# Optimization experiments

Measured on AMD Instinct MI355X. Metric: run time of the kernel, lower is better.

## Reference

```python
import jax, jax.numpy as jnp
import numpy as np
import math

D_MODEL = 1024
D_STATE = 16
D_CONV = 4
EXPAND = 2
D_INNER = EXPAND * D_MODEL  # 2048
DT_RANK = 64
B_SZ = 2
L_SEQ = 1024


def setup_inputs() -> dict:
    key = jax.random.key(0)
    ks = jax.random.split(key, 10)
    x = jax.random.normal(ks[0], (B_SZ, L_SEQ, D_MODEL), dtype=jnp.float32)
    in_proj_w = jax.random.normal(ks[1], (2 * D_INNER, D_MODEL), dtype=jnp.float32) * (1.0 / math.sqrt(D_MODEL))
    conv_w = jax.random.normal(ks[2], (D_INNER, 1, D_CONV), dtype=jnp.float32) * (1.0 / math.sqrt(D_CONV))
    conv_b = jax.random.normal(ks[3], (D_INNER,), dtype=jnp.float32) * 0.01
    x_proj_w = jax.random.normal(ks[4], (DT_RANK + 2 * D_STATE, D_INNER), dtype=jnp.float32) * (1.0 / math.sqrt(D_INNER))
    dt_init_std = DT_RANK ** (-0.5)
    dt_proj_w = jax.random.uniform(ks[5], (D_INNER, DT_RANK), dtype=jnp.float32, minval=-dt_init_std, maxval=dt_init_std)
    dt = jnp.exp(jax.random.uniform(ks[6], (D_INNER,), dtype=jnp.float32) * (math.log(0.1) - math.log(0.001)) + math.log(0.001))
    dt = jnp.clip(dt, 1e-4, None)
    dt_proj_b = dt + jnp.log(-jnp.expm1(-dt))
    A_log = jnp.log(jnp.tile(jnp.arange(1, D_STATE + 1, dtype=jnp.float32)[None, :], (D_INNER, 1)))
    D = jnp.ones((D_INNER,), dtype=jnp.float32)
    out_proj_w = jax.random.normal(ks[7], (D_MODEL, D_INNER), dtype=jnp.float32) * (1.0 / math.sqrt(D_INNER))
    return {"x": x, "in_proj_w": in_proj_w, "conv_w": conv_w, "conv_b": conv_b,
            "x_proj_w": x_proj_w, "dt_proj_w": dt_proj_w, "dt_proj_b": dt_proj_b,
            "A_log": A_log, "D": D, "out_proj_w": out_proj_w}


def _mamba_forward(x, in_proj_w, conv_w, conv_b, x_proj_w, dt_proj_w, dt_proj_b, A_log, D, out_proj_w):
    B, L, _ = x.shape
    # input projection -> x, z each [B, L, Di]
    xz = jnp.einsum('bld,ed->ble', x, in_proj_w)
    xs, z = jnp.split(xz, 2, axis=-1)
    # causal depthwise conv along L (torch pads K-1 both sides then trims -> left pad only)
    xc = jnp.transpose(xs, (0, 2, 1))  # [B, Di, L]
    xc = jax.lax.conv_general_dilated(
        xc, conv_w, window_strides=(1,), padding=[(D_CONV - 1, 0)],
        feature_group_count=D_INNER, dimension_numbers=('NCH', 'OIH', 'NCH'))
    xc = xc + conv_b[None, :, None]
    xs = jnp.transpose(xc, (0, 2, 1))  # [B, L, Di]
    xs = jax.nn.silu(xs)
    # SSM parameters
    A = -jnp.exp(A_log)  # [Di, N]
    dbc = jnp.einsum('bld,ed->ble', xs, x_proj_w)
    delta_r = dbc[..., :DT_RANK]
    Bm = dbc[..., DT_RANK:DT_RANK + D_STATE]       # [B, L, N]
    Cm = dbc[..., DT_RANK + D_STATE:]              # [B, L, N]
    delta = jnp.einsum('blr,dr->bld', delta_r, dt_proj_w)
    delta = jax.nn.softplus(delta + dt_proj_b)     # [B, L, Di]
    # selective scan: h_t = exp(delta*A)*h_{t-1} + delta*B*x
    dA = jnp.exp(delta[..., None] * A)                          # [B, L, Di, N]
    dBx = (delta * xs)[..., None] * Bm[:, :, None, :]           # [B, L, Di, N]
    dA_t = jnp.moveaxis(dA, 1, 0)    # [L, B, Di, N]
    dBx_t = jnp.moveaxis(dBx, 1, 0)
    C_t = jnp.moveaxis(Cm, 1, 0)     # [L, B, N]
    h0 = jnp.zeros((B, D_INNER, D_STATE), dtype=xs.dtype)

    def step(h, inp):
        da, bx, c = inp
        h = da * h + bx
        y = jnp.einsum('bdn,bn->bd', h, c)
        return h, y

    _, ys = jax.lax.scan(step, h0, (dA_t, dBx_t, C_t))
    y = jnp.moveaxis(ys, 0, 1)       # [B, L, Di]
    y = y + D * xs
    # gating and output projection
    out = y * jax.nn.silu(z)
    return jnp.einsum('bld,od->blo', out, out_proj_w)


def reference(x, in_proj_w, conv_w, conv_b, x_proj_w, dt_proj_w, dt_proj_b, A_log, D, out_proj_w):
    return _mamba_forward(x, in_proj_w, conv_w, conv_b, x_proj_w, dt_proj_w, dt_proj_b, A_log, D, out_proj_w)
```

## Files before the change

### kernel.cpp

```cpp
#include <hip/hip_runtime.h>
#include <hip/hip_bf16.h>

typedef __attribute__((ext_vector_type(8))) short short8;
typedef __attribute__((ext_vector_type(4))) float f32x4;
typedef __hip_bfloat16 bf16;

#define D_MODEL 1024
#define D_INNER 2048
#define DT_RANK 64
#define D_STATE 16
#define B_SZ 2
#define L_SEQ 1024
#define NSEG 32
#define SL 32

__device__ __forceinline__ float b2f(bf16 x){ return __bfloat162float(x); }
__device__ __forceinline__ bf16  f2b(float x){ return __float2bfloat16(x); }

__device__ __forceinline__ void cvt_store8(bf16* dst, const float* s){
  union { short8 v; bf16 e[8]; } u;
  #pragma unroll
  for (int i = 0; i < 8; i++) u.e[i] = f2b(s[i]);
  *(short8*)dst = u.v;
}

__device__ __forceinline__ void gl_lds16(const bf16* g, bf16* l){
  __builtin_amdgcn_global_load_lds((const __attribute__((address_space(1))) unsigned int*)g,
                                   (__attribute__((address_space(3))) unsigned int*)l, 16, 0, 0);
}

__global__ __launch_bounds__(256) void cvt5_k(const float* s0, bf16* d0, int c0,
                                              const float* s1, bf16* d1, int c1,
                                              const float* s2, bf16* d2, int c2,
                                              const float* s3, bf16* d3, int c3,
                                              const float* s4, bf16* d4, int c4)
{
  int i = blockIdx.x * 256 + threadIdx.x;
  const float* s; bf16* d; int off;
  if      (i < c0) { s = s0; d = d0; off = i; }
  else if (i < c1) { s = s1; d = d1; off = i - c0; }
  else if (i < c2) { s = s2; d = d2; off = i - c1; }
  else if (i < c3) { s = s3; d = d3; off = i - c2; }
  else if (i < c4) { s = s4; d = d4; off = i - c3; }
  else return;
  float b[8];
  *(float4*)&b[0] = *(const float4*)(s + (size_t)off * 8);
  *(float4*)&b[4] = *(const float4*)(s + (size_t)off * 8 + 4);
  cvt_store8(d + (size_t)off * 8, b);
}

template<int MODE, int JT>
__global__ __launch_bounds__(256) void gemm_glds(const bf16* __restrict__ A,
                                                 const bf16* __restrict__ B,
                                                 void* __restrict__ Cout,
                                                 int M, int N, int K)
{
  constexpr int BN = JT * 32;
  constexpr int BI = BN / 64;
  constexpr int ES = (MODE == 0) ? 4 : 2;
  static_assert(BN * ES == 256, "copy-out assumes 256B tile rows");
  constexpr int ROWB = BN * ES + 16;
  constexpr int STAGE_AB = 128*32*2 + BN*32*2;
  constexpr int SMEM = (128 * ROWB > STAGE_AB) ? 128 * ROWB : STAGE_AB;
  __shared__ __align__(16) char smem[SMEM];
  bf16* As = (bf16*)smem;
  bf16* Bs = (bf16*)(smem + 128*32*2);

  const int bm = blockIdx.y * 128, bn = blockIdx.x * BN;
  const int tid  = threadIdx.x;
  const int lane = tid & 63, wave = tid >> 6;
  const int wm = (wave & 1) * 64, wn = (wave >> 1) * (JT * 16);
  const int r = lane & 15, q = lane >> 4;

  const bf16* asrc[2];
  #pragma unroll
  for (int i = 0; i < 2; i++) {
    int c = i * 256 + tid;
    asrc[i] = A + (size_t)(bm + (c >> 2)) * K + (c & 3) * 8;
  }
  const bf16* bsrc[BI];
  #pragma unroll
  for (int i = 0; i < BI; i++) {
    int c = i * 256 + tid;
    bsrc[i] = B + (size_t)(bn + (c >> 2)) * K + (c & 3) * 8;
  }

  f32x4 acc[4][JT];
  #pragma unroll
  for (int i = 0; i < 4; i++)
    #pragma unroll
    for (int j = 0; j < JT; j++) acc[i][j] = (f32x4){0.f,0.f,0.f,0.f};

  for (int k0 = 0; k0 < K; k0 += 32) {
    #pragma unroll
    for (int i = 0; i < 2; i++)
      gl_lds16(asrc[i] + k0, &As[(i * 256 + tid) * 8]);
    #pragma unroll
    for (int i = 0; i < BI; i++)
      gl_lds16(bsrc[i] + k0, &Bs[(i * 256 + tid) * 8]);
    __syncthreads();
    short8 af[4], bfr[JT];
    #pragma unroll
    for (int i = 0; i < 4; i++)  af[i]  = *(const short8*)&As[(wm + i*16 + r) * 32 + q*8];
    #pragma unroll
    for (int j = 0; j < JT; j++) bfr[j] = *(const short8*)&Bs[(wn + j*16 + r) * 32 + q*8];
    #pragma unroll
    for (int j = 0; j < JT; j++)
      #pragma unroll
      for (int i = 0; i < 4; i++)
        acc[i][j] = __builtin_amdgcn_mfma_f32_16x16x32_bf16(af[i], bfr[j], acc[i][j], 0, 0, 0);
    __syncthreads();
  }

  #pragma unroll
  for (int i = 0; i < 4; i++)
    #pragma unroll
    for (int j = 0; j < JT; j++)
      #pragma unroll
      for (int t = 0; t < 4; t++) {
        int lrow = wm + i*16 + q*4 + t;
        int lcol = wn + j*16 + r;
        float v = acc[i][j][t];
        if (MODE == 0) *(float*)(smem + lrow*ROWB + lcol*4) = v;
        else           *(bf16*)(smem + lrow*ROWB + lcol*2) = f2b(v);
      }
  __syncthreads();
  {
    int row0 = tid >> 3, ch = tid & 7;
    #pragma unroll
    for (int rr = 0; rr < 4; rr++) {
      int row = row0 + rr * 32;
      const char* src = smem + row*ROWB + ch*32;
      float4 w0 = *(const float4*)src;
      float4 w1 = *(const float4*)(src + 16);
      char* gdst = (char*)Cout + ((size_t)(bm + row) * N + bn) * ES + ch*32;
      *(float4*)gdst        = w0;
      *(float4*)(gdst + 16) = w1;
    }
  }
}

__global__ __launch_bounds__(256) void gemm_dt(const bf16* __restrict__ A,
                                               const bf16* __restrict__ W,
                                               float* __restrict__ Cout,
                                               const float* __restrict__ bias,
                                               int M, int N)
{
  __shared__ __align__(16) float stg[4][16][68];
  const int lane = threadIdx.x & 63, wave = threadIdx.x >> 6;
  const int ntg  = N >> 6;
  const int task = blockIdx.x * 4 + wave;
  const int mt   = task / ntg;
  const int ng   = task - mt * ntg;
  const int r = lane & 15, q = lane >> 4;

  const bf16* pa = A + (size_t)(mt*16 + r) * DT_RANK + q*8;
  short8 a0 = *(const short8*)pa;
  short8 a1 = *(const short8*)(pa + 32);

  #pragma unroll
  for (int j = 0; j < 4; j++) {
    const bf16* pb = W + (size_t)(ng*64 + j*16 + r) * DT_RANK + q*8;
    short8 b0 = *(const short8*)pb;
    short8 b1 = *(const short8*)(pb + 32);
    f32x4 c = {0.f,0.f,0.f,0.f};
    c = __builtin_amdgcn_mfma_f32_16x16x32_bf16(a0, b0, c, 0, 0, 0);
    c = __builtin_amdgcn_mfma_f32_16x16x32_bf16(a1, b1, c, 0, 0, 0);
    float bv = bias[ng*64 + j*16 + r];
    #pragma unroll
    for (int t = 0; t < 4; t++) {
      float xv = c[t] + bv;
      float sp = (xv > 20.f) ? xv : log1pf(__expf(xv));
      stg[wave][q*4 + t][j*16 + r] = sp;
    }
  }
  {
    int row = lane >> 2, q4 = lane & 3;
    const float* src = &stg[wave][row][q4 * 16];
    float4 w0 = *(const float4*)(src);
    float4 w1 = *(const float4*)(src + 4);
    float4 w2 = *(const float4*)(src + 8);
    float4 w3 = *(const float4*)(src + 12);
    float* gdst = Cout + (size_t)(mt*16 + row) * N + ng*64 + q4*16;
    *(float4*)(gdst)      = w0;
    *(float4*)(gdst + 4)  = w1;
    *(float4*)(gdst + 8)  = w2;
    *(float4*)(gdst + 12) = w3;
  }
}

__global__ __launch_bounds__(256) void gemm_xproj(const bf16* __restrict__ A,
                                                  const bf16* __restrict__ W,
                                                  float* __restrict__ dbc,
                                                  bf16* __restrict__ dr)
{
  const int K = D_INNER;
  const int lane = threadIdx.x & 63, wave = threadIdx.x >> 6;
  const int mt = blockIdx.y * 4 + wave;
  const int nt = blockIdx.x;
  const int r = lane & 15, q = lane >> 4;
  const bf16* pa = A + (size_t)(mt*16 + r) * K + q*8;
  const bf16* pb = W + (size_t)(nt*16 + r) * K + q*8;
  f32x4 a0 = {0.f,0.f,0.f,0.f}, a1 = a0, a2 = a0, a3 = a0;
  for (int k0 = 0; k0 < K; k0 += 128) {
    short8 x0 = *(const short8*)(pa + k0);
    short8 w0 = *(const short8*)(pb + k0);
    short8 x1 = *(const short8*)(pa + k0 + 32);
    short8 w1 = *(const short8*)(pb + k0 + 32);
    short8 x2 = *(const short8*)(pa + k0 + 64);
    short8 w2 = *(const short8*)(pb + k0 + 64);
    short8 x3 = *(const short8*)(pa + k0 + 96);
    short8 w3 = *(const short8*)(pb + k0 + 96);
    a0 = __builtin_amdgcn_mfma_f32_16x16x32_bf16(x0, w0, a0, 0, 0, 0);
    a1 = __builtin_amdgcn_mfma_f32_16x16x32_bf16(x1, w1, a1, 0, 0, 0);
    a2 = __builtin_amdgcn_mfma_f32_16x16x32_bf16(x2, w2, a2, 0, 0, 0);
    a3 = __builtin_amdgcn_mfma_f32_16x16x32_bf16(x3, w3, a3, 0, 0, 0);
  }
  f32x4 acc = (a0 + a1) + (a2 + a3);
  #pragma unroll
  for (int t = 0; t < 4; t++) {
    int row = mt*16 + q*4 + t;
    int col = nt*16 + r;
    dbc[(size_t)row * 96 + col] = acc[t];
    if (col < DT_RANK) dr[(size_t)row * DT_RANK + col] = f2b(acc[t]);
  }
}

__global__ __launch_bounds__(256) void conv_silu_k(const bf16* __restrict__ xz,
                                                   const float* __restrict__ cw,
                                                   const float* __restrict__ cb,
                                                   bf16* __restrict__ xs_b)
{
  int idx = blockIdx.x * 256 + threadIdx.x;
  int dg = idx & (D_INNER/8 - 1);
  int bl = idx >> 8;
  int l  = bl & (L_SEQ - 1);
  int d0 = dg * 8;
  const float4* cw4 = (const float4*)cw;
  float4 w[8];
  #pragma unroll
  for (int i = 0; i < 8; i++) w[i] = cw4[d0 + i];
  float acc[8];
  #pragma unroll
  for (int i = 0; i < 8; i++) acc[i] = cb[d0 + i];
  #pragma unroll
  for (int j = 0; j < 4; ++j) {
    int lp = l - 3 + j;
    if (lp >= 0) {
      short8 v = *(const short8*)(xz + (size_t)(bl - 3 + j) * (2*D_INNER) + d0);
      #pragma unroll
      for (int i = 0; i < 8; i++)
        acc[i] += ((const float*)&w[i])[j] * b2f(((const bf16*)&v)[i]);
    }
  }
  float o[8];
  #pragma unroll
  for (int i = 0; i < 8; i++) o[i] = acc[i] / (1.f + __expf(-acc[i]));
  cvt_store8(xs_b + (size_t)idx * 8, o);
}

__global__ __launch_bounds__(256) void scan_pass1(const float* __restrict__ delta,
                                                  const bf16* __restrict__ xs,
                                                  const float* __restrict__ dbc,
                                                  const float* __restrict__ A_log,
                                                  float* __restrict__ hseg,
                                                  float* __restrict__ Stot)
{
  __shared__ float bcs[SL][32];
  const int d   = blockIdx.x * 256 + threadIdx.x;
  const int seg = blockIdx.y, b = blockIdx.z;
  for (int i = threadIdx.x; i < SL*32; i += 256) {
    int l = i >> 5, c = i & 31;
    bcs[l][c] = dbc[((size_t)b*L_SEQ + seg*SL + l)*96 + DT_RANK + c];
  }
  __syncthreads();
  float An[16], h[16];
  #pragma unroll
  for (int n = 0; n < 16; n++) { An[n] = -__expf(A_log[d*16 + n]); h[n] = 0.f; }
  float S = 0.f;
  for (int li = 0; li < SL; ++li) {
    size_t bl = (size_t)b * L_SEQ + seg*SL + li;
    float dv = delta[bl*D_INNER + d];
    float xv = b2f(xs[bl*D_INNER + d]);
    S += dv;
    float dx = dv * xv;
    #pragma unroll
    for (int n = 0; n < 16; n++)
      h[n] = __expf(dv * An[n]) * h[n] + dx * bcs[li][n];
  }
  float* hp = hseg + (((size_t)seg*B_SZ + b)*D_INNER + d) * 16;
  #pragma unroll
  for (int n = 0; n < 16; n++) hp[n] = h[n];
  Stot[((size_t)seg*B_SZ + b)*D_INNER + d] = S;
}

__global__ __launch_bounds__(256) void scan_combine(const float* __restrict__ Stot,
                                                    float* __restrict__ hseg,
                                                    const float* __restrict__ A_log)
{
  int idx = blockIdx.x * 256 + threadIdx.x;
  int n = idx & 15;
  int d = (idx >> 4) & (D_INNER - 1);
  int b = idx >> 15;
  float An = -__expf(A_log[d*16 + n]);
  float H = 0.f;
  for (int s = 0; s < NSEG; s++) {
    size_t base = ((size_t)s*B_SZ + b)*D_INNER + d;
    float St   = Stot[base];
    float hloc = hseg[base*16 + n];
    hseg[base*16 + n] = H;
    H = __expf(An*St)*H + hloc;
  }
}

__global__ __launch_bounds__(256) void scan_pass3(const float* __restrict__ delta,
                                                  const bf16* __restrict__ xs,
                                                  const float* __restrict__ dbc,
                                                  const float* __restrict__ A_log,
                                                  const float* __restrict__ hseg,
                                                  const bf16* __restrict__ xz,
                                                  const float* __restrict__ Dw,
                                                  bf16* __restrict__ outin)
{
  __shared__ float bcs[SL][32];
  const int d   = blockIdx.x * 256 + threadIdx.x;
  const int seg = blockIdx.y, b = blockIdx.z;
  for (int i = threadIdx.x; i < SL*32; i += 256) {
    int l = i >> 5, c = i & 31;
    bcs[l][c] = dbc[((size_t)b*L_SEQ + seg*SL + l)*96 + DT_RANK + c];
  }
  __syncthreads();
  float An[16], h[16];
  const float* hp = hseg + (((size_t)seg*B_SZ + b)*D_INNER + d) * 16;
  #pragma unroll
  for (int n = 0; n < 16; n++) { An[n] = -__expf(A_log[d*16 + n]); h[n] = hp[n]; }
  const float Dv = Dw[d];
  for (int li = 0; li < SL; ++li) {
    size_t bl = (size_t)b * L_SEQ + seg*SL + li;
    float dv = delta[bl*D_INNER + d];
    float xv = b2f(xs[bl*D_INNER + d]);
    float dx = dv * xv;
    float y = 0.f;
    #pragma unroll
    for (int n = 0; n < 16; n++) {
      h[n] = __expf(dv * An[n]) * h[n] + dx * bcs[li][n];
      y   += h[n] * bcs[li][16 + n];
    }
    y += Dv * xv;
    float z = b2f(xz[bl*(size_t)(2*D_INNER) + D_INNER + d]);
    float g = z / (1.f + __expf(-z));
    outin[bl*D_INNER + d] = f2b(y * g);
  }
}

extern "C" void kernel_launch(void* const* d_in, const int* in_sizes, int n_in,
                              void* d_out, int out_size, void* d_ws, size_t ws_size,
                              hipStream_t stream)
{
  const float* x      = (const float*)d_in[0];
  const float* in_w   = (const float*)d_in[1];
  const float* conv_w = (const float*)d_in[2];
  const float* conv_b = (const float*)d_in[3];
  const float* xp_w   = (const float*)d_in[4];
  const float* dt_w   = (const float*)d_in[5];
  const float* dt_b   = (const float*)d_in[6];
  const float* A_log  = (const float*)d_in[7];
  const float* Dw     = (const float*)d_in[8];
  const float* out_w  = (const float*)d_in[9];
  float* out = (float*)d_out;

  char* p = (char*)d_ws;
  bf16*  xz    = (bf16*)p;  p += (size_t)B_SZ*L_SEQ*2*D_INNER*2;
  bf16*  xs_b  = (bf16*)p;  p += (size_t)B_SZ*L_SEQ*D_INNER*2;
  float* dbc   = (float*)p; p += (size_t)B_SZ*L_SEQ*96*4;
  bf16*  dr    = (bf16*)p;  p += (size_t)B_SZ*L_SEQ*DT_RANK*2;
  float* delta = (float*)p; p += (size_t)B_SZ*L_SEQ*D_INNER*4;
  float* Stot  = (float*)p; p += (size_t)NSEG*B_SZ*D_INNER*4;
  bf16*  outin = (bf16*)p;  p += (size_t)B_SZ*L_SEQ*D_INNER*2;
  bf16*  xp_wb = (bf16*)p;  p += (size_t)(DT_RANK+2*D_STATE)*D_INNER*2;
  bf16*  dt_wb = (bf16*)p;  p += (size_t)D_INNER*DT_RANK*2;
  bf16*  ow_b  = (bf16*)p;  p += (size_t)D_MODEL*D_INNER*2;
  char* u = p;
  bf16*  xb    = (bf16*)u;
  bf16*  in_wb = (bf16*)(u + (size_t)B_SZ*L_SEQ*D_MODEL*2);
  float* hseg  = (float*)u;
  p += (size_t)B_SZ*L_SEQ*(D_MODEL + 2*D_INNER)*2;

  const int M = B_SZ * L_SEQ;

  cvt5_k<<<4256, 256, 0, stream>>>(x, xb, 262144,
                                   in_w, in_wb, 786432,
                                   xp_w, xp_wb, 811008,
                                   dt_w, dt_wb, 827392,
                                   out_w, ow_b, 1089536);
  gemm_glds<2,4><<<dim3(2*D_INNER/128, M/128), 256, 0, stream>>>(xb, in_wb, xz, M, 2*D_INNER, D_MODEL);
  conv_silu_k<<<(M*D_INNER/8)/256, 256, 0, stream>>>(xz, conv_w, conv_b, xs_b);
  gemm_xproj<<<dim3(6, M/64), 256, 0, stream>>>(xs_b, xp_wb, dbc, dr);
  gemm_dt<<<(M/16)*(D_INNER/64)/4, 256, 0, stream>>>(dr, dt_wb, delta, dt_b, M, D_INNER);
  scan_pass1<<<dim3(D_INNER/256, NSEG, B_SZ), 256, 0, stream>>>(delta, xs_b, dbc, A_log, hseg, Stot);
  scan_combine<<<(B_SZ*D_INNER*16)/256, 256, 0, stream>>>(Stot, hseg, A_log);
  scan_pass3<<<dim3(D_INNER/256, NSEG, B_SZ), 256, 0, stream>>>(delta, xs_b, dbc, A_log, hseg, xz, Dw, outin);
  gemm_glds<0,2><<<dim3(D_MODEL/64, M/128), 256, 0, stream>>>(outin, ow_b, out, M, D_MODEL, D_INNER);
}
```

Baseline: 268.8 us.

## Split-K the output projection, swizzle GEMM tiles, and narrow in_proj tiles

The output-projection GEMM now splits K across two grid slices that write fp32 partials, and a new add kernel sums them. This doubles the number of workgroups on a small M×N output. The GEMM also gains a block-index swizzle meant to improve L2 reuse, and the in-projection tile width drops from 128 to 64 columns to launch more blocks. The LDS-staged coalesced copy-out is replaced with direct per-element global stores, which gives up write coalescing. The split also adds an extra partial-buffer round trip and one more kernel launch.

```diff
diff --git a/kernel.cpp b/kernel.cpp
--- a/kernel.cpp
+++ b/kernel.cpp
@@ -49,7 +49,7 @@
   cvt_store8(d + (size_t)off * 8, b);
 }
 
-template<int MODE, int JT>
+template<int MODE, int JT, int SPLITK>
 __global__ __launch_bounds__(256) void gemm_glds(const bf16* __restrict__ A,
                                                  const bf16* __restrict__ B,
                                                  void* __restrict__ Cout,
@@ -57,16 +57,18 @@
 {
   constexpr int BN = JT * 32;
   constexpr int BI = BN / 64;
-  constexpr int ES = (MODE == 0) ? 4 : 2;
-  static_assert(BN * ES == 256, "copy-out assumes 256B tile rows");
-  constexpr int ROWB = BN * ES + 16;
-  constexpr int STAGE_AB = 128*32*2 + BN*32*2;
-  constexpr int SMEM = (128 * ROWB > STAGE_AB) ? 128 * ROWB : STAGE_AB;
-  __shared__ __align__(16) char smem[SMEM];
-  bf16* As = (bf16*)smem;
-  bf16* Bs = (bf16*)(smem + 128*32*2);
-
-  const int bm = blockIdx.y * 128, bn = blockIdx.x * BN;
+  __shared__ bf16 As[128 * 32];
+  __shared__ bf16 Bs[BN * 32];
+
+  const int gx = gridDim.x;
+  const int nwg = gx * gridDim.y;
+  const int flat = blockIdx.y * gx + blockIdx.x;
+  const int swz = (flat & 7) * (nwg >> 3) + (flat >> 3);
+  const int bm = (swz / gx) * 128, bn = (swz % gx) * BN;
+
+  const int Kc = K / SPLITK;
+  const int kb = (SPLITK > 1) ? blockIdx.z * Kc : 0;
+
   const int tid  = threadIdx.x;
   const int lane = tid & 63, wave = tid >> 6;
   const int wm = (wave & 1) * 64, wn = (wave >> 1) * (JT * 16);
@@ -76,13 +78,13 @@
   #pragma unroll
   for (int i = 0; i < 2; i++) {
     int c = i * 256 + tid;
-    asrc[i] = A + (size_t)(bm + (c >> 2)) * K + (c & 3) * 8;
+    asrc[i] = A + (size_t)(bm + (c >> 2)) * K + kb + (c & 3) * 8;
   }
   const bf16* bsrc[BI];
   #pragma unroll
   for (int i = 0; i < BI; i++) {
     int c = i * 256 + tid;
-    bsrc[i] = B + (size_t)(bn + (c >> 2)) * K + (c & 3) * 8;
+    bsrc[i] = B + (size_t)(bn + (c >> 2)) * K + kb + (c & 3) * 8;
   }
 
   f32x4 acc[4][JT];
@@ -91,7 +93,7 @@
     #pragma unroll
     for (int j = 0; j < JT; j++) acc[i][j] = (f32x4){0.f,0.f,0.f,0.f};
 
-  for (int k0 = 0; k0 < K; k0 += 32) {
+  for (int k0 = 0; k0 < Kc; k0 += 32) {
     #pragma unroll
     for (int i = 0; i < 2; i++)
       gl_lds16(asrc[i] + k0, &As[(i * 256 + tid) * 8]);
@@ -112,32 +114,29 @@
     __syncthreads();
   }
 
+  float* outf = (float*)Cout + (size_t)((SPLITK > 1) ? blockIdx.z : 0) * M * N;
   #pragma unroll
   for (int i = 0; i < 4; i++)
     #pragma unroll
     for (int j = 0; j < JT; j++)
       #pragma unroll
       for (int t = 0; t < 4; t++) {
-        int lrow = wm + i*16 + q*4 + t;
-        int lcol = wn + j*16 + r;
+        int row = bm + wm + i*16 + q*4 + t;
+        int col = bn + wn + j*16 + r;
         float v = acc[i][j][t];
-        if (MODE == 0) *(float*)(smem + lrow*ROWB + lcol*4) = v;
-        else           *(bf16*)(smem + lrow*ROWB + lcol*2) = f2b(v);
+        if (MODE == 0) outf[(size_t)row * N + col] = v;
+        else           ((bf16*)Cout)[(size_t)row * N + col] = f2b(v);
       }
-  __syncthreads();
-  {
-    int row0 = tid >> 3, ch = tid & 7;
-    #pragma unroll
-    for (int rr = 0; rr < 4; rr++) {
-      int row = row0 + rr * 32;
-      const char* src = smem + row*ROWB + ch*32;
-      float4 w0 = *(const float4*)src;
-      float4 w1 = *(const float4*)(src + 16);
-      char* gdst = (char*)Cout + ((size_t)(bm + row) * N + bn) * ES + ch*32;
-      *(float4*)gdst        = w0;
-      *(float4*)(gdst + 16) = w1;
-    }
-  }
+}
+
+__global__ __launch_bounds__(256) void addout_k(const float* __restrict__ p,
+                                                float* __restrict__ out, int n4)
+{
+  int i = blockIdx.x * 256 + threadIdx.x;
+  float4 a = ((const float4*)p)[i];
+  float4 b = ((const float4*)p)[(size_t)i + n4];
+  float4 o; o.x = a.x + b.x; o.y = a.y + b.y; o.z = a.z + b.z; o.w = a.w + b.w;
+  ((float4*)out)[i] = o;
 }
 
 __global__ __launch_bounds__(256) void gemm_dt(const bf16* __restrict__ A,
@@ -380,6 +379,7 @@
   bf16*  xp_wb = (bf16*)p;  p += (size_t)(DT_RANK+2*D_STATE)*D_INNER*2;
   bf16*  dt_wb = (bf16*)p;  p += (size_t)D_INNER*DT_RANK*2;
   bf16*  ow_b  = (bf16*)p;  p += (size_t)D_MODEL*D_INNER*2;
+  float* out_p = (float*)p; p += (size_t)2*B_SZ*L_SEQ*D_MODEL*4;
   char* u = p;
   bf16*  xb    = (bf16*)u;
   bf16*  in_wb = (bf16*)(u + (size_t)B_SZ*L_SEQ*D_MODEL*2);
@@ -393,12 +393,13 @@
                                    xp_w, xp_wb, 811008,
                                    dt_w, dt_wb, 827392,
                                    out_w, ow_b, 1089536);
-  gemm_glds<2,4><<<dim3(2*D_INNER/128, M/128), 256, 0, stream>>>(xb, in_wb, xz, M, 2*D_INNER, D_MODEL);
+  gemm_glds<2,2,1><<<dim3(2*D_INNER/64, M/128, 1), 256, 0, stream>>>(xb, in_wb, xz, M, 2*D_INNER, D_MODEL);
   conv_silu_k<<<(M*D_INNER/8)/256, 256, 0, stream>>>(xz, conv_w, conv_b, xs_b);
   gemm_xproj<<<dim3(6, M/64), 256, 0, stream>>>(xs_b, xp_wb, dbc, dr);
   gemm_dt<<<(M/16)*(D_INNER/64)/4, 256, 0, stream>>>(dr, dt_wb, delta, dt_b, M, D_INNER);
   scan_pass1<<<dim3(D_INNER/256, NSEG, B_SZ), 256, 0, stream>>>(delta, xs_b, dbc, A_log, hseg, Stot);
   scan_combine<<<(B_SZ*D_INNER*16)/256, 256, 0, stream>>>(Stot, hseg, A_log);
   scan_pass3<<<dim3(D_INNER/256, NSEG, B_SZ), 256, 0, stream>>>(delta, xs_b, dbc, A_log, hseg, xz, Dw, outin);
-  gemm_glds<0,2><<<dim3(D_MODEL/64, M/128), 256, 0, stream>>>(outin, ow_b, out, M, D_MODEL, D_INNER);
-}
+  gemm_glds<0,2,2><<<dim3(D_MODEL/64, M/128, 2), 256, 0, stream>>>(outin, ow_b, out_p, M, D_MODEL, D_INNER);
+  addout_k<<<(M*D_MODEL/4)/256, 256, 0, stream>>>(out_p, out, M*D_MODEL/4);
+}
```

Measured after the change: 261.4 us. 2.8% less time.
